# Kernel tuning notes

Measured on AMD Instinct MI355X. Metric: run time of the kernel, lower is better.

## Reference

```python
import jax, jax.numpy as jnp
import numpy as np

VOCAB = 30522
EMBED = 768
NUM_CAT = 18
HIS = 50
CLICK_DIM = 100


def setup_inputs() -> dict:
    key = jax.random.key(0)
    ks = jax.random.split(key, 12)
    B, H, S = 64, HIS, 32
    encoding = jax.random.randint(ks[0], (B, H, S), 0, VOCAB)
    attention_mask = jnp.ones((B, H, S), dtype=bool)
    category_mask = jax.random.randint(ks[1], (B, NUM_CAT, H), 0, 2).astype(bool)
    inv = 1.0 / np.sqrt(EMBED)
    return {
        "encoding": encoding,
        "attention_mask": attention_mask,
        "category_mask": category_mask,
        "word_emb": jax.random.normal(ks[2], (VOCAB, EMBED), jnp.float32) * 0.02,
        "proj_w": jax.random.normal(ks[3], (EMBED, EMBED), jnp.float32) * inv,
        "proj_b": jnp.zeros((EMBED,), jnp.float32),
        "category_embedding": jax.random.normal(ks[4], (NUM_CAT, EMBED), jnp.float32) * 0.02,
        "w_news_attn": jax.random.normal(ks[5], (EMBED,), jnp.float32) * inv,
        "w_cat_attn": jax.random.normal(ks[6], (EMBED,), jnp.float32) * inv,
        "num_click_emb": jax.random.normal(ks[7], (HIS + 1, CLICK_DIM), jnp.float32) * 0.02,
        "click_w": jax.random.normal(ks[8], (CLICK_DIM,), jnp.float32) * (1.0 / np.sqrt(CLICK_DIM)),
        "click_b": jnp.zeros((), jnp.float32),
    }


def reference(encoding, attention_mask, category_mask, word_emb, proj_w, proj_b,
              category_embedding, w_news_attn, w_cat_attn, num_click_emb, click_w, click_b):
    # --- news_encoder stand-in: embedding lookup + masked mean pool + tanh(Linear) ---
    tok = word_emb[encoding]                                   # [B,H,S,E]
    m = attention_mask.astype(tok.dtype)[..., None]            # [B,H,S,1]
    pooled = (tok * m).sum(axis=2) / jnp.maximum(m.sum(axis=2), 1.0)  # [B,H,E]
    news_repr = jnp.tanh(pooled @ proj_w + proj_b)             # [B,H,E]

    # --- per-category masked softmax attention over history ---
    news_w = news_repr @ w_news_attn                           # [B,H]
    neg_inf = jnp.float32(-jnp.inf)
    scores = jnp.where(category_mask, news_w[:, None, :], neg_inf)  # [B,C,H]
    attn = jnp.nan_to_num(jax.nn.softmax(scores, axis=-1))     # nan rows (empty cats) -> 0
    category_interest = jnp.einsum('bch,bhe->bce', attn, news_repr)  # [B,C,E]
    category_repr = category_interest + category_embedding     # [B,C,E]

    # --- category-level attention with num-click scoring ---
    cat_w = category_repr @ w_cat_attn                          # [B,C]
    count = category_mask.sum(axis=-1).astype(jnp.int32)        # [B,C], <= HIS
    click_score = num_click_emb[count] @ click_w + click_b      # [B,C]
    final = cat_w + click_score
    final = jnp.where(count == 0, neg_inf, final)
    final = jax.nn.softmax(final, axis=-1)                      # [B,C]
    user_repr = jnp.einsum('bc,bce->be', final, category_repr)  # [B,E]
    return category_repr, user_repr
```

## Files before the change

kernel.cpp:

```cpp
#include <hip/hip_runtime.h>
#include <hip/hip_bf16.h>
#include <math.h>

#define VOCAB 30522
#define EMBED 768
#define NUM_CAT 18
#define HIS 50
#define SEQ 32
#define BATCH 64
#define CLICK_DIM 100

typedef short v8s __attribute__((ext_vector_type(8)));
typedef float v4f __attribute__((ext_vector_type(4)));
typedef unsigned short v8u __attribute__((ext_vector_type(8)));
typedef unsigned char v8c __attribute__((ext_vector_type(8)));

#define OFF_POOLED 0
#define OFF_WT     4915200
#define OFF_NR     6094848
#define OFF_NEWSW  15925248
#define OFF_FLAG   16177664
#define OFF_QTAB   16252928
#define OFF_DSCALE 39693824
#define WS_NEED    39815912ull

__device__ __forceinline__ bool read_mask(const void* p, int i, int flag) {
    if (flag == 0) return ((const int*)p)[i] != 0;
    if (flag == 1) return ((const unsigned char*)p)[i] != 0;
    return ((const float*)p)[i] != 0.0f;
}

__device__ __forceinline__ float bf2f(unsigned short u) {
    union { unsigned int i; float f; } cv;
    cv.i = ((unsigned int)u) << 16;
    return cv.f;
}
__device__ __forceinline__ unsigned short f2bf(float f) {
    __hip_bfloat16 h = __float2bfloat16(f);
    return *(unsigned short*)&h;
}

__global__ __launch_bounds__(256) void kprep(
        const float* __restrict__ W, __hip_bfloat16* __restrict__ Wt,
        const unsigned int* __restrict__ cm, int* __restrict__ flag_out,
        const float* __restrict__ wemb, signed char* __restrict__ qtab,
        float* __restrict__ dscales, float* __restrict__ news_w) {
    int blk = blockIdx.x;
    if (blk < 576) {
        __shared__ float t[32][33];
        int tx = threadIdx.x & 31, ty = threadIdx.x >> 5;
        int k0 = (blk % 24) * 32, n0 = (blk / 24) * 32;
        #pragma unroll
        for (int i = 0; i < 4; ++i)
            t[ty + i * 8][tx] = W[(size_t)(k0 + ty + i * 8) * EMBED + n0 + tx];
        __syncthreads();
        #pragma unroll
        for (int i = 0; i < 4; ++i)
            Wt[(size_t)(n0 + ty + i * 8) * EMBED + k0 + tx] =
                __float2bfloat16(t[tx][ty + i * 8]);
    } else if (blk == 576) {
        __shared__ int word_gt1, byte_gt1;
        if (threadIdx.x == 0) { word_gt1 = 0; byte_gt1 = 0; }
        __syncthreads();
        int lw = 0, lb = 0;
        for (int i = threadIdx.x; i < 14400; i += 256) {
            unsigned int v = cm[i];
            if (v > 1u) lw = 1;
            if ((v & 0xFFu) > 1u || ((v >> 8) & 0xFFu) > 1u ||
                ((v >> 16) & 0xFFu) > 1u || ((v >> 24) & 0xFFu) > 1u) lb = 1;
        }
        if (lw) atomicOr(&word_gt1, 1);
        if (lb) atomicOr(&byte_gt1, 1);
        for (int i = threadIdx.x; i < BATCH * HIS; i += 256) news_w[i] = 0.f;
        __syncthreads();
        if (threadIdx.x == 0) {
            int f = 0;
            if (word_gt1) f = byte_gt1 ? 2 : 1;
            *flag_out = f;
        }
    } else {
        __shared__ float red[4];
        int row = blk - 577;
        int tid = threadIdx.x, lane = tid & 63, wv = tid >> 6;
        float4 v = make_float4(0.f, 0.f, 0.f, 0.f);
        if (tid < 192)
            v = *(const float4*)(wemb + (size_t)row * EMBED + tid * 4);
        float mx = fmaxf(fmaxf(fabsf(v.x), fabsf(v.y)),
                         fmaxf(fabsf(v.z), fabsf(v.w)));
        #pragma unroll
        for (int off = 32; off; off >>= 1) mx = fmaxf(mx, __shfl_xor(mx, off));
        if (lane == 0) red[wv] = mx;
        __syncthreads();
        float rowmax = fmaxf(fmaxf(red[0], red[1]), red[2]);
        if (tid < 192) {
            float inv = (rowmax > 0.f) ? 127.0f / rowmax : 0.f;
            int q0 = __float2int_rn(v.x * inv);
            int q1 = __float2int_rn(v.y * inv);
            int q2 = __float2int_rn(v.z * inv);
            int q3 = __float2int_rn(v.w * inv);
            q0 = max(-127, min(127, q0)); q1 = max(-127, min(127, q1));
            q2 = max(-127, min(127, q2)); q3 = max(-127, min(127, q3));
            char4 c; c.x = (signed char)q0; c.y = (signed char)q1;
            c.z = (signed char)q2; c.w = (signed char)q3;
            *(char4*)(qtab + (size_t)row * EMBED + tid * 4) = c;
        }
        if (tid == 0) dscales[row] = rowmax * (1.0f / 127.0f);
    }
}

__global__ __launch_bounds__(192) void k1c_pool(
        const int* __restrict__ enc, const void* amask,
        const unsigned char* __restrict__ qtab, const float* __restrict__ dscales,
        __hip_bfloat16* __restrict__ pooled, const int* __restrict__ flagp) {
    int tid = threadIdx.x, lane = tid & 63;
    int blk = blockIdx.x;
    int flag = *flagp;
    int bh0 = blk * 2, bh1 = blk * 2 + 1;
    bool mm = (lane < 32) ? read_mask(amask, bh0 * SEQ + lane, flag)
                          : read_mask(amask, bh1 * SEQ + (lane - 32), flag);
    unsigned long long bal = __ballot(mm);
    unsigned int mb0 = (unsigned int)(bal & 0xFFFFFFFFull);
    unsigned int mb1 = (unsigned int)(bal >> 32);
    int half = (tid >= 96) ? 1 : 0;
    int bh = half ? bh1 : bh0;
    unsigned int mb = half ? mb1 : mb0;
    float cnt = (float)__popc(mb);
    int slot = tid - half * 96;
    const int* e = enc + bh * SEQ;
    float a[8] = {};
    v8c v[8], w[8];
    float ds[8], dw[8];
    #pragma unroll
    for (int j = 0; j < 8; ++j) {
        int tok = e[j];
        v[j] = ((const v8c*)(qtab + (size_t)tok * EMBED))[slot];
        ds[j] = dscales[tok];
    }
    #pragma unroll
    for (int s0 = 0; s0 < SEQ; s0 += 8) {
        if (s0 + 8 < SEQ) {
            #pragma unroll
            for (int j = 0; j < 8; ++j) {
                int tok = e[s0 + 8 + j];
                w[j] = ((const v8c*)(qtab + (size_t)tok * EMBED))[slot];
                dw[j] = dscales[tok];
            }
        }
        #pragma unroll
        for (int j = 0; j < 8; ++j) {
            float msc = ((mb >> (s0 + j)) & 1u) ? ds[j] : 0.f;
            #pragma unroll
            for (int k = 0; k < 8; ++k) {
                int q = (int)(signed char)v[j][k];
                a[k] = fmaf((float)q, msc, a[k]);
            }
        }
        #pragma unroll
        for (int j = 0; j < 8; ++j) { v[j] = w[j]; ds[j] = dw[j]; }
    }
    float d = 1.0f / fmaxf(cnt, 1.0f);
    v8u o;
    #pragma unroll
    for (int k = 0; k < 8; ++k) o[k] = f2bf(a[k] * d);
    *(v8u*)(((unsigned short*)pooled) + (size_t)bh * EMBED + slot * 8) = o;
}

__global__ __launch_bounds__(1024) void k0_detect(
        const unsigned int* __restrict__ cm, int* flag_out, float* __restrict__ news_w) {
    __shared__ int word_gt1, byte_gt1;
    if (threadIdx.x == 0) { word_gt1 = 0; byte_gt1 = 0; }
    __syncthreads();
    int lw = 0, lb = 0;
    for (int i = threadIdx.x; i < 14400; i += blockDim.x) {
        unsigned int v = cm[i];
        if (v > 1u) lw = 1;
        if ((v & 0xFFu) > 1u || ((v >> 8) & 0xFFu) > 1u ||
            ((v >> 16) & 0xFFu) > 1u || ((v >> 24) & 0xFFu) > 1u) lb = 1;
    }
    if (lw) atomicOr(&word_gt1, 1);
    if (lb) atomicOr(&byte_gt1, 1);
    for (int i = threadIdx.x; i < BATCH * HIS; i += blockDim.x) news_w[i] = 0.f;
    __syncthreads();
    if (threadIdx.x == 0) {
        int f = 0;
        if (word_gt1) f = byte_gt1 ? 2 : 1;
        *flag_out = f;
    }
}

__global__ __launch_bounds__(256) void k2a_wt(
        const float* __restrict__ W, __hip_bfloat16* __restrict__ Wt) {
    __shared__ float t[32][33];
    int tx = threadIdx.x & 31, ty = threadIdx.x >> 5;
    int k0 = blockIdx.x * 32, n0 = blockIdx.y * 32;
    #pragma unroll
    for (int i = 0; i < 4; ++i)
        t[ty + i * 8][tx] = W[(size_t)(k0 + ty + i * 8) * EMBED + n0 + tx];
    __syncthreads();
    #pragma unroll
    for (int i = 0; i < 4; ++i)
        Wt[(size_t)(n0 + ty + i * 8) * EMBED + k0 + tx] =
            __float2bfloat16(t[tx][ty + i * 8]);
}

__global__ __launch_bounds__(192) void k1_pool(
        const int* __restrict__ enc, const void* amask,
        const float* __restrict__ wemb, __hip_bfloat16* __restrict__ pooled,
        const int* __restrict__ flagp) {
    int wave = threadIdx.x >> 6, lane = threadIdx.x & 63;
    int bh = blockIdx.x;
    int flag = *flagp;
    const int* e = enc + bh * SEQ;
    bool m = (lane < SEQ) ? read_mask(amask, bh * SEQ + lane, flag) : false;
    unsigned long long mb = __ballot(m);
    float cnt = (float)__popcll(mb);
    int fslot = wave * 64 + lane;
    float ax = 0.f, ay = 0.f, az = 0.f, aw = 0.f;
    #pragma unroll
    for (int s0 = 0; s0 < SEQ; s0 += 8) {
        float4 v[8];
        #pragma unroll
        for (int j = 0; j < 8; ++j)
            v[j] = ((const float4*)(wemb + (size_t)e[s0 + j] * EMBED))[fslot];
        #pragma unroll
        for (int j = 0; j < 8; ++j) {
            float mmv = ((mb >> (s0 + j)) & 1ull) ? 1.0f : 0.0f;
            ax += mmv * v[j].x; ay += mmv * v[j].y;
            az += mmv * v[j].z; aw += mmv * v[j].w;
        }
    }
    float d = 1.0f / fmaxf(cnt, 1.0f);
    ushort4 pk;
    pk.x = f2bf(ax * d); pk.y = f2bf(ay * d);
    pk.z = f2bf(az * d); pk.w = f2bf(aw * d);
    *(ushort4*)((unsigned short*)pooled + (size_t)bh * EMBED + fslot * 4) = pk;
}

#define BM 64
#define BN 64
#define GBK 64
#define LDP 72
__global__ __launch_bounds__(256) void k2_mfma(
        const __hip_bfloat16* __restrict__ A,
        const __hip_bfloat16* __restrict__ Bt,
        const float* __restrict__ bias,
        const float* __restrict__ wna,
        unsigned short* __restrict__ C,
        float* __restrict__ news_w) {
    __shared__ short As[BM * LDP];
    __shared__ short Bs[BN * LDP];
    int tid = threadIdx.x;
    int wave = tid >> 6, lane = tid & 63;
    int l15 = lane & 15, l4 = lane >> 4;
    int wr = wave >> 1, wc = wave & 1;
    int row0 = blockIdx.x * BM;
    int col0 = blockIdx.y * BN;
    v4f acc[2][2] = {};

    int ra[2], ca[2];
    #pragma unroll
    for (int it = 0; it < 2; ++it) {
        int chunk = tid + it * 256;
        ra[it] = chunk >> 3; ca[it] = chunk & 7;
    }

    v8s pa[2], pb[2];
    #pragma unroll
    for (int it = 0; it < 2; ++it) {
        pa[it] = *(const v8s*)(A  + (size_t)(row0 + ra[it]) * EMBED + ca[it] * 8);
        pb[it] = *(const v8s*)(Bt + (size_t)(col0 + ra[it]) * EMBED + ca[it] * 8);
    }

    for (int s = 0; s < EMBED / GBK; ++s) {
        #pragma unroll
        for (int it = 0; it < 2; ++it) {
            *(v8s*)&As[ra[it] * LDP + ca[it] * 8] = pa[it];
            *(v8s*)&Bs[ra[it] * LDP + ca[it] * 8] = pb[it];
        }
        __syncthreads();
        if (s < EMBED / GBK - 1) {
            int k0 = (s + 1) * GBK;
            #pragma unroll
            for (int it = 0; it < 2; ++it) {
                pa[it] = *(const v8s*)(A  + (size_t)(row0 + ra[it]) * EMBED + k0 + ca[it] * 8);
                pb[it] = *(const v8s*)(Bt + (size_t)(col0 + ra[it]) * EMBED + k0 + ca[it] * 8);
            }
        }
        #pragma unroll
        for (int kk = 0; kk < 2; ++kk) {
            v8s af[2], bf_[2];
            #pragma unroll
            for (int mi = 0; mi < 2; ++mi)
                af[mi] = *(const v8s*)&As[(wr * 32 + mi * 16 + l15) * LDP + kk * 32 + l4 * 8];
            #pragma unroll
            for (int ni = 0; ni < 2; ++ni)
                bf_[ni] = *(const v8s*)&Bs[(wc * 32 + ni * 16 + l15) * LDP + kk * 32 + l4 * 8];
            #pragma unroll
            for (int mi = 0; mi < 2; ++mi)
                #pragma unroll
                for (int ni = 0; ni < 2; ++ni)
                    acc[mi][ni] = __builtin_amdgcn_mfma_f32_16x16x32_bf16(
                        af[mi], bf_[ni], acc[mi][ni], 0, 0, 0);
        }
        __syncthreads();
    }
    float bcol[2], wcol[2];
    #pragma unroll
    for (int ni = 0; ni < 2; ++ni) {
        int col = col0 + wc * 32 + ni * 16 + l15;
        bcol[ni] = bias[col]; wcol[ni] = wna[col];
    }
    #pragma unroll
    for (int mi = 0; mi < 2; ++mi) {
        #pragma unroll
        for (int r = 0; r < 4; ++r) {
            int row = row0 + wr * 32 + mi * 16 + l4 * 4 + r;
            float pr = 0.f;
            #pragma unroll
            for (int ni = 0; ni < 2; ++ni) {
                int col = col0 + wc * 32 + ni * 16 + l15;
                float tv = tanhf(acc[mi][ni][r] + bcol[ni]);
                C[(size_t)row * EMBED + col] = f2bf(tv);
                pr += tv * wcol[ni];
            }
            pr += __shfl_xor(pr, 1); pr += __shfl_xor(pr, 2);
            pr += __shfl_xor(pr, 4); pr += __shfl_xor(pr, 8);
            if (l15 == 0) atomicAdd(&news_w[row], pr);
        }
    }
}

__global__ __launch_bounds__(768) void k4_fused(
        const void* cmask, const unsigned short* __restrict__ nr,
        const float* __restrict__ news_w, const float* __restrict__ cat_emb,
        const float* __restrict__ w_cat, const float* __restrict__ click_emb,
        const float* __restrict__ click_w, const float* __restrict__ click_b,
        float* __restrict__ out_cat, float* __restrict__ user,
        const int* __restrict__ flagp) {
    int b = blockIdx.x, tid = threadIdx.x;
    int wave = tid >> 6, lane = tid & 63;
    int flag = *flagp;
    __shared__ float plds[HIS][20];
    __shared__ float redbuf[NUM_CAT][12];
    __shared__ float clicks[NUM_CAT];
    __shared__ int   cnts[NUM_CAT];
    __shared__ float logit[NUM_CAT];

    for (int c = wave; c < NUM_CAT; c += 12) {
        bool m = false; float v = -INFINITY;
        if (lane < HIS) {
            m = read_mask(cmask, (b * NUM_CAT + c) * HIS + lane, flag);
            if (m) v = news_w[b * HIS + lane];
        }
        unsigned long long bal = __ballot(m);
        int cnt = __popcll(bal);
        float maxv = v;
        #pragma unroll
        for (int off = 32; off; off >>= 1) maxv = fmaxf(maxv, __shfl_xor(maxv, off));
        float e = (v == -INFINITY) ? 0.f : expf(v - maxv);
        float sum = e;
        #pragma unroll
        for (int off = 32; off; off >>= 1) sum += __shfl_xor(sum, off);
        if (lane < HIS)
            plds[lane][c] = (cnt == 0 || v == -INFINITY) ? 0.f : e / sum;
        float cs = 0.f;
        if (lane < HIS) {
            const float* ce = click_emb + (size_t)cnt * CLICK_DIM;
            cs = ce[lane] * click_w[lane] + ce[lane + HIS] * click_w[lane + HIS];
        }
        #pragma unroll
        for (int off = 32; off; off >>= 1) cs += __shfl_down(cs, off);
        if (lane == 0) { cnts[c] = cnt; clicks[c] = cs + click_b[0]; }
    }
    __syncthreads();

    int col = tid;
    const unsigned short* nrb = nr + (size_t)b * HIS * EMBED;
    float acc[NUM_CAT];
    #pragma unroll
    for (int c = 0; c < NUM_CAT; ++c) acc[c] = 0.f;
    #pragma unroll 5
    for (int h = 0; h < HIS; ++h) {
        float v = bf2f(nrb[h * EMBED + col]);
        #pragma unroll
        for (int c = 0; c < NUM_CAT; ++c) acc[c] += plds[h][c] * v;
    }
    float part[NUM_CAT];
    float wv = w_cat[col];
    float* ocb = out_cat + (size_t)b * NUM_CAT * EMBED;
    #pragma unroll
    for (int c = 0; c < NUM_CAT; ++c) {
        float o = acc[c] + cat_emb[c * EMBED + col];
        acc[c] = o;
        ocb[c * EMBED + col] = o;
        part[c] = o * wv;
    }
    #pragma unroll
    for (int c = 0; c < NUM_CAT; ++c) {
        float s = part[c];
        #pragma unroll
        for (int off = 32; off; off >>= 1) s += __shfl_down(s, off);
        if (lane == 0) redbuf[c][wave] = s;
    }
    __syncthreads();
    if (tid < NUM_CAT) {
        float s = 0.f;
        #pragma unroll
        for (int w = 0; w < 12; ++w) s += redbuf[tid][w];
        logit[tid] = (cnts[tid] == 0) ? -INFINITY : (s + clicks[tid]);
    }
    __syncthreads();

    float maxv = -INFINITY;
    #pragma unroll
    for (int c = 0; c < NUM_CAT; ++c) maxv = fmaxf(maxv, logit[c]);
    float sum = 0.f;
    #pragma unroll
    for (int c = 0; c < NUM_CAT; ++c)
        sum += (logit[c] == -INFINITY) ? 0.f : expf(logit[c] - maxv);
    float u = 0.f;
    #pragma unroll
    for (int c = 0; c < NUM_CAT; ++c) {
        float w = (logit[c] == -INFINITY) ? 0.f : expf(logit[c] - maxv) / sum;
        u += w * acc[c];
    }
    user[(size_t)b * EMBED + col] = u;
}

extern "C" void kernel_launch(void* const* d_in, const int* in_sizes, int n_in,
                              void* d_out, int out_size, void* d_ws, size_t ws_size,
                              hipStream_t stream) {
    const int*   enc    = (const int*)d_in[0];
    const void*  amask  = d_in[1];
    const void*  cmask  = d_in[2];
    const float* wemb   = (const float*)d_in[3];
    const float* projw  = (const float*)d_in[4];
    const float* projb  = (const float*)d_in[5];
    const float* catemb = (const float*)d_in[6];
    const float* wna    = (const float*)d_in[7];
    const float* wca    = (const float*)d_in[8];
    const float* clemb  = (const float*)d_in[9];
    const float* clw    = (const float*)d_in[10];
    const float* clb    = (const float*)d_in[11];

    unsigned char* wsb = (unsigned char*)d_ws;
    __hip_bfloat16* pooled = (__hip_bfloat16*)(wsb + OFF_POOLED);
    __hip_bfloat16* Wt     = (__hip_bfloat16*)(wsb + OFF_WT);
    unsigned short* nr     = (unsigned short*)(wsb + OFF_NR);
    float* news_w = (float*)(wsb + OFF_NEWSW);
    int*   flag   = (int*)(wsb + OFF_FLAG);
    signed char* qtab = (signed char*)(wsb + OFF_QTAB);
    float* dscales = (float*)(wsb + OFF_DSCALE);

    float* out_cat = (float*)d_out;
    float* user    = (float*)d_out + BATCH * NUM_CAT * EMBED;

    if (ws_size >= WS_NEED) {
        kprep<<<577 + VOCAB, 256, 0, stream>>>(
            projw, Wt, (const unsigned int*)cmask, flag, wemb, qtab, dscales, news_w);
        k1c_pool<<<1600, 192, 0, stream>>>(enc, amask, (const unsigned char*)qtab,
                                           dscales, pooled, flag);
    } else {
        k0_detect<<<1, 1024, 0, stream>>>((const unsigned int*)cmask, flag, news_w);
        dim3 gt(24, 24);
        k2a_wt<<<gt, 256, 0, stream>>>(projw, Wt);
        k1_pool<<<3200, 192, 0, stream>>>(enc, amask, wemb, pooled, flag);
    }
    dim3 g2(50, 12);
    k2_mfma<<<g2, 256, 0, stream>>>(pooled, Wt, projb, wna, nr, news_w);
    k4_fused<<<BATCH, 768, 0, stream>>>(cmask, nr, news_w, catemb, wca,
                                        clemb, clw, clb, out_cat, user, flag);
}
```

Measured before the change: 76.59 us.

## Split category attention kernel into column-parallel stage and user-softmax stage

Replaces the single per-batch fused category/user kernel with two kernels. The first splits each batch's 768 embedding columns across three blocks, computes the per-category softmax weights and click scores, and writes category representations while accumulating category logits through atomics into workspace. The second kernel does the category softmax and the weighted user sum. The aim is to fill more compute units than the previous 64-block grid, at the cost of an extra launch, atomics, and re-reading out_cat.

```diff
diff --git a/kernel.cpp b/kernel.cpp
--- a/kernel.cpp
+++ b/kernel.cpp
@@ -22,7 +22,10 @@
 #define OFF_FLAG   16177664
 #define OFF_QTAB   16252928
 #define OFF_DSCALE 39693824
-#define WS_NEED    39815912ull
+#define OFF_LOGACC 39815936
+#define OFF_CLICKS 39820544
+#define OFF_CNTS   39825152
+#define WS_NEED    39829760ull
 
 __device__ __forceinline__ bool read_mask(const void* p, int i, int flag) {
     if (flag == 0) return ((const int*)p)[i] != 0;
@@ -44,7 +47,8 @@
         const float* __restrict__ W, __hip_bfloat16* __restrict__ Wt,
         const unsigned int* __restrict__ cm, int* __restrict__ flag_out,
         const float* __restrict__ wemb, signed char* __restrict__ qtab,
-        float* __restrict__ dscales, float* __restrict__ news_w) {
+        float* __restrict__ dscales, float* __restrict__ news_w,
+        float* __restrict__ logacc) {
     int blk = blockIdx.x;
     if (blk < 576) {
         __shared__ float t[32][33];
@@ -72,6 +76,7 @@
         if (lw) atomicOr(&word_gt1, 1);
         if (lb) atomicOr(&byte_gt1, 1);
         for (int i = threadIdx.x; i < BATCH * HIS; i += 256) news_w[i] = 0.f;
+        for (int i = threadIdx.x; i < BATCH * NUM_CAT; i += 256) logacc[i] = 0.f;
         __syncthreads();
         if (threadIdx.x == 0) {
             int f = 0;
@@ -330,6 +335,112 @@
     }
 }
 
+__global__ __launch_bounds__(256) void k4a_cat(
+        const void* cmask, const unsigned short* __restrict__ nr,
+        const float* __restrict__ news_w, const float* __restrict__ cat_emb,
+        const float* __restrict__ w_cat, const float* __restrict__ click_emb,
+        const float* __restrict__ click_w, const float* __restrict__ click_b,
+        float* __restrict__ out_cat, float* __restrict__ logacc,
+        float* __restrict__ clicks_ws, int* __restrict__ cnts_ws,
+        const int* __restrict__ flagp) {
+    int blk = blockIdx.x;
+    int b = blk / 3, third = blk % 3;
+    int tid = threadIdx.x, wave = tid >> 6, lane = tid & 63;
+    int flag = *flagp;
+    __shared__ float plds[HIS][20];
+    __shared__ float redbuf[NUM_CAT][4];
+
+    for (int c = wave; c < NUM_CAT; c += 4) {
+        bool m = false; float v = -INFINITY;
+        if (lane < HIS) {
+            m = read_mask(cmask, (b * NUM_CAT + c) * HIS + lane, flag);
+            if (m) v = news_w[b * HIS + lane];
+        }
+        unsigned long long bal = __ballot(m);
+        int cnt = __popcll(bal);
+        float maxv = v;
+        #pragma unroll
+        for (int off = 32; off; off >>= 1) maxv = fmaxf(maxv, __shfl_xor(maxv, off));
+        float e = (v == -INFINITY) ? 0.f : expf(v - maxv);
+        float sum = e;
+        #pragma unroll
+        for (int off = 32; off; off >>= 1) sum += __shfl_xor(sum, off);
+        if (lane < HIS)
+            plds[lane][c] = (cnt == 0 || v == -INFINITY) ? 0.f : e / sum;
+        if (third == 0) {
+            float cs = 0.f;
+            if (lane < HIS) {
+                const float* ce = click_emb + (size_t)cnt * CLICK_DIM;
+                cs = ce[lane] * click_w[lane] + ce[lane + HIS] * click_w[lane + HIS];
+            }
+            #pragma unroll
+            for (int off = 32; off; off >>= 1) cs += __shfl_down(cs, off);
+            if (lane == 0) {
+                cnts_ws[b * NUM_CAT + c] = cnt;
+                clicks_ws[b * NUM_CAT + c] = cs + click_b[0];
+            }
+        }
+    }
+    __syncthreads();
+
+    int col = third * 256 + tid;
+    const unsigned short* nrb = nr + (size_t)b * HIS * EMBED;
+    float acc[NUM_CAT];
+    #pragma unroll
+    for (int c = 0; c < NUM_CAT; ++c) acc[c] = 0.f;
+    #pragma unroll 5
+    for (int h = 0; h < HIS; ++h) {
+        float v = bf2f(nrb[h * EMBED + col]);
+        #pragma unroll
+        for (int c = 0; c < NUM_CAT; ++c) acc[c] += plds[h][c] * v;
+    }
+    float wv = w_cat[col];
+    float* ocb = out_cat + (size_t)b * NUM_CAT * EMBED;
+    #pragma unroll
+    for (int c = 0; c < NUM_CAT; ++c) {
+        float o = acc[c] + cat_emb[c * EMBED + col];
+        ocb[c * EMBED + col] = o;
+        float s = o * wv;
+        #pragma unroll
+        for (int off = 32; off; off >>= 1) s += __shfl_down(s, off);
+        if (lane == 0) redbuf[c][wave] = s;
+    }
+    __syncthreads();
+    if (tid < NUM_CAT) {
+        float s = redbuf[tid][0] + redbuf[tid][1] + redbuf[tid][2] + redbuf[tid][3];
+        atomicAdd(&logacc[b * NUM_CAT + tid], s);
+    }
+}
+
+__global__ __launch_bounds__(768) void k4b_user(
+        const float* __restrict__ logacc, const float* __restrict__ clicks_ws,
+        const int* __restrict__ cnts_ws, const float* __restrict__ out_cat,
+        float* __restrict__ user) {
+    int b = blockIdx.x, tid = threadIdx.x;
+    __shared__ float logit[NUM_CAT];
+    if (tid < NUM_CAT) {
+        int cnt = cnts_ws[b * NUM_CAT + tid];
+        logit[tid] = (cnt == 0) ? -INFINITY
+                     : (logacc[b * NUM_CAT + tid] + clicks_ws[b * NUM_CAT + tid]);
+    }
+    __syncthreads();
+    float maxv = -INFINITY;
+    #pragma unroll
+    for (int c = 0; c < NUM_CAT; ++c) maxv = fmaxf(maxv, logit[c]);
+    float sum = 0.f;
+    #pragma unroll
+    for (int c = 0; c < NUM_CAT; ++c)
+        sum += (logit[c] == -INFINITY) ? 0.f : expf(logit[c] - maxv);
+    const float* ocb = out_cat + (size_t)b * NUM_CAT * EMBED;
+    float u = 0.f;
+    #pragma unroll
+    for (int c = 0; c < NUM_CAT; ++c) {
+        float w = (logit[c] == -INFINITY) ? 0.f : expf(logit[c] - maxv) / sum;
+        u += w * ocb[c * EMBED + tid];
+    }
+    user[(size_t)b * EMBED + tid] = u;
+}
+
 __global__ __launch_bounds__(768) void k4_fused(
         const void* cmask, const unsigned short* __restrict__ nr,
         const float* __restrict__ news_w, const float* __restrict__ cat_emb,
@@ -451,23 +562,33 @@
     int*   flag   = (int*)(wsb + OFF_FLAG);
     signed char* qtab = (signed char*)(wsb + OFF_QTAB);
     float* dscales = (float*)(wsb + OFF_DSCALE);
+    float* logacc  = (float*)(wsb + OFF_LOGACC);
+    float* clicks  = (float*)(wsb + OFF_CLICKS);
+    int*   cnts    = (int*)(wsb + OFF_CNTS);
 
     float* out_cat = (float*)d_out;
     float* user    = (float*)d_out + BATCH * NUM_CAT * EMBED;
 
     if (ws_size >= WS_NEED) {
         kprep<<<577 + VOCAB, 256, 0, stream>>>(
-            projw, Wt, (const unsigned int*)cmask, flag, wemb, qtab, dscales, news_w);
+            projw, Wt, (const unsigned int*)cmask, flag, wemb, qtab, dscales,
+            news_w, logacc);
         k1c_pool<<<1600, 192, 0, stream>>>(enc, amask, (const unsigned char*)qtab,
                                            dscales, pooled, flag);
+        dim3 g2(50, 12);
+        k2_mfma<<<g2, 256, 0, stream>>>(pooled, Wt, projb, wna, nr, news_w);
+        k4a_cat<<<BATCH * 3, 256, 0, stream>>>(cmask, nr, news_w, catemb, wca,
+                                               clemb, clw, clb, out_cat, logacc,
+                                               clicks, cnts, flag);
+        k4b_user<<<BATCH, 768, 0, stream>>>(logacc, clicks, cnts, out_cat, user);
     } else {
         k0_detect<<<1, 1024, 0, stream>>>((const unsigned int*)cmask, flag, news_w);
         dim3 gt(24, 24);
         k2a_wt<<<gt, 256, 0, stream>>>(projw, Wt);
         k1_pool<<<3200, 192, 0, stream>>>(enc, amask, wemb, pooled, flag);
-    }
-    dim3 g2(50, 12);
-    k2_mfma<<<g2, 256, 0, stream>>>(pooled, Wt, projb, wna, nr, news_w);
-    k4_fused<<<BATCH, 768, 0, stream>>>(cmask, nr, news_w, catemb, wca,
-                                        clemb, clw, clb, out_cat, user, flag);
-}
+        dim3 g2(50, 12);
+        k2_mfma<<<g2, 256, 0, stream>>>(pooled, Wt, projb, wna, nr, news_w);
+        k4_fused<<<BATCH, 768, 0, stream>>>(cmask, nr, news_w, catemb, wca,
+                                            clemb, clw, clb, out_cat, user, flag);
+    }
+}
```

Result: slower. 97.08 us (+26.8%).
